# Kernel tuning notes

Hardware: AMD Instinct MI355X
Metric: run time of the kernel (lower is better)

The kernel has to match this reference:

```python
import jax, jax.numpy as jnp
import numpy as np

# dims: N batch, L seq, H heads, d projection_dim, P position_dimension
N, Lq, Lk, H, d, P = 2, 1024, 1024, 8, 64, 1
D = H * d


def _kernel(x):
    # _log_exp_kernel: positive feature map log(1+exp(x)) (softplus)
    return jax.nn.softplus(x)


def setup_inputs() -> dict:
    key = jax.random.key(0)
    ks = jax.random.split(key, 8)
    sc = 1.0 / np.sqrt(D).astype(np.float32)
    return {
        "query": jax.random.normal(ks[0], (N, Lq, D), jnp.float32),
        "key_seq": jax.random.normal(ks[1], (N, Lk, D), jnp.float32),
        "Wq": jax.random.normal(ks[2], (D, D), jnp.float32) * sc,
        "Wk": jax.random.normal(ks[3], (D, D), jnp.float32) * sc,
        "Wv": jax.random.normal(ks[4], (D, D), jnp.float32) * sc,
        "position_coeffs": jax.random.uniform(ks[5], (H, d), jnp.float32, 0.5, 1.5),
        "position_weight": jax.random.normal(ks[6], (H, d, P), jnp.float32) * 1e-3,
        "position_bias": jax.random.normal(ks[7], (H, d), jnp.float32) * 1e-2,
    }


def reference(query, key_seq, Wq, Wk, Wv, position_coeffs, position_weight, position_bias):
    # torch Linear (no bias): y = x @ W.T
    q = _kernel(jnp.einsum('nld,ed->nle', query, Wq).reshape(N, Lq, H, d))
    k = _kernel(jnp.einsum('nld,ed->nle', key_seq, Wk).reshape(N, Lk, H, d))
    v = jnp.einsum('nld,ed->nle', key_seq, Wv).reshape(N, Lk, H, d)
    # (N, H, L, d)
    q = jnp.transpose(q, (0, 2, 1, 3))
    k = jnp.transpose(k, (0, 2, 1, 3))
    v = jnp.transpose(v, (0, 2, 1, 3))

    # default positions: arange, query_offset = 0
    qpos = jnp.broadcast_to(jnp.arange(Lq, dtype=jnp.float32).reshape(1, Lq, 1), (N, Lq, P))
    kpos = jnp.broadcast_to(jnp.arange(Lk, dtype=jnp.float32).reshape(1, Lk, 1), (N, Lk, P))
    pq = jnp.einsum('nlp,hkp->nhlk', qpos, position_weight) + position_bias[None, :, None, :]
    pk = jnp.einsum('nlp,hkp->nhlk', kpos, position_weight)

    coeff = position_coeffs[None, :, None, :]  # (1, H, 1, d)

    def part(f, values):
        # causal (mask_future) linear attention via inclusive cumsum over keys
        Qf = q * f(pq) * coeff           # (N, H, Lq, d)
        Kf = k * f(pk)                   # (N, H, Lk, d)
        S = jnp.cumsum(jnp.einsum('nhkd,nhke->nhkde', Kf, values), axis=2)
        return jnp.einsum('nhqd,nhqde->nhqe', Qf, S)

    num = part(jnp.cos, v) + part(jnp.sin, v)           # (N, H, Lq, d)
    unit = jnp.ones((N, H, Lk, 1), jnp.float32)
    den = part(jnp.cos, unit) + part(jnp.sin, unit)     # (N, H, Lq, 1)
    attn = num / den
    return jnp.transpose(attn, (0, 2, 1, 3)).reshape(N, Lq, D)
```

## Files before the change

kernel.cpp:

```cpp
#include <hip/hip_runtime.h>
#include <cmath>

#define NB    2
#define LSEQ  1024
#define NH    8
#define HD    64
#define DD    512
#define FDIM  128
#define EV    65
#define SEP   80
#define CHUNK 64
#define NC    16
#define NBH   16

typedef short short8 __attribute__((ext_vector_type(8)));
typedef float floatx4 __attribute__((ext_vector_type(4)));
typedef unsigned short ushort;

__device__ __forceinline__ float softplusf(float x) {
  return fmaxf(x, 0.0f) + log1pf(expf(-fabsf(x)));
}

__device__ __forceinline__ ushort f2bf(float f) {
  unsigned u = __float_as_uint(f);
  u += 0x7fffu + ((u >> 16) & 1u);
  return (ushort)(u >> 16);
}

__device__ __forceinline__ short8 cvt8(float4 a, float4 b) {
  short8 r;
  r[0] = (short)f2bf(a.x); r[1] = (short)f2bf(a.y);
  r[2] = (short)f2bf(a.z); r[3] = (short)f2bf(a.w);
  r[4] = (short)f2bf(b.x); r[5] = (short)f2bf(b.y);
  r[6] = (short)f2bf(b.z); r[7] = (short)f2bf(b.w);
  return r;
}

__global__ __launch_bounds__(256) void k_proj(
    const float* __restrict__ Xq, const float* __restrict__ Xkv,
    const float* __restrict__ Wq, const float* __restrict__ Wk,
    const float* __restrict__ Wv, const float* __restrict__ pw,
    const float* __restrict__ pb, const float* __restrict__ pc,
    ushort* __restrict__ Qfb, ushort* __restrict__ Kfb,
    ushort* __restrict__ Vxb)
{
  __shared__ short Al[2][64][72];
  __shared__ short Bl[2][64][72];
  const int b = blockIdx.x;
  int m0, e0, pmode;
  const float *X, *W;
  if (b < 256) {
    m0 = (b >> 3) << 6; e0 = (b & 7) << 6;
    X = Xq; W = Wq + (size_t)e0 * DD; pmode = 0;
  } else {
    const int bb = b - 256;
    m0 = (bb >> 4) << 6;
    const int nt = bb & 15;
    e0 = (nt & 7) << 6;
    X = Xkv;
    if (nt < 8) { W = Wk + (size_t)e0 * DD; pmode = 1; }
    else        { W = Wv + (size_t)e0 * DD; pmode = 2; }
  }
  const int tid  = threadIdx.x;
  const int r    = tid >> 2;
  const int ko   = (tid & 3) << 4;
  const int wave = tid >> 6, lane = tid & 63;
  const int quad = lane >> 4, lm = lane & 15;
  const float* Ag = X + (size_t)(m0 + r) * DD + ko;
  const float* Bg = W + (size_t)r * DD + ko;
  float4 a[4], bb4[4];
#pragma unroll
  for (int u = 0; u < 4; ++u) {
    a[u]   = *(const float4*)(Ag + (u << 2));
    bb4[u] = *(const float4*)(Bg + (u << 2));
  }
  *(short8*)&Al[0][r][ko]     = cvt8(a[0], a[1]);
  *(short8*)&Al[0][r][ko + 8] = cvt8(a[2], a[3]);
  *(short8*)&Bl[0][r][ko]     = cvt8(bb4[0], bb4[1]);
  *(short8*)&Bl[0][r][ko + 8] = cvt8(bb4[2], bb4[3]);
  __syncthreads();

  floatx4 acc[4] = {};
  for (int k0 = 0; k0 < DD; k0 += 64) {
    const int cur  = (k0 >> 6) & 1;
    const bool more = (k0 + 64 < DD);
    if (more) {
#pragma unroll
      for (int u = 0; u < 4; ++u) {
        a[u]   = *(const float4*)(Ag + k0 + 64 + (u << 2));
        bb4[u] = *(const float4*)(Bg + k0 + 64 + (u << 2));
      }
    }
#pragma unroll
    for (int ks = 0; ks < 2; ++ks) {
      const short8 af = *(const short8*)&Al[cur][(wave << 4) + lm][(quad << 3) + (ks << 5)];
#pragma unroll
      for (int t = 0; t < 4; ++t) {
        const short8 bf = *(const short8*)&Bl[cur][(t << 4) + lm][(quad << 3) + (ks << 5)];
        acc[t] = __builtin_amdgcn_mfma_f32_16x16x32_bf16(af, bf, acc[t], 0, 0, 0);
      }
    }
    if (more) {
      const int nxt = cur ^ 1;
      *(short8*)&Al[nxt][r][ko]     = cvt8(a[0], a[1]);
      *(short8*)&Al[nxt][r][ko + 8] = cvt8(a[2], a[3]);
      *(short8*)&Bl[nxt][r][ko]     = cvt8(bb4[0], bb4[1]);
      *(short8*)&Bl[nxt][r][ko + 8] = cvt8(bb4[2], bb4[3]);
    }
    __syncthreads();
  }
#pragma unroll
  for (int t = 0; t < 4; ++t) {
    const int e = e0 + (t << 4) + lm;
    const int h = e >> 6, jj = e & 63;
    if (pmode == 2) {
#pragma unroll
      for (int rg = 0; rg < 4; ++rg) {
        const int m = m0 + (wave << 4) + (quad << 2) + rg;
        const int n = m >> 10, l = m & 1023;
        Vxb[((size_t)(n * NH + h) * LSEQ + l) * HD + jj] = f2bf(acc[t][rg]);
      }
    } else {
      const float pwv = pw[e];
      const float pbv = (pmode == 0) ? pb[e] : 0.0f;
      const float pcv = (pmode == 0) ? pc[e] : 1.0f;
      ushort* base = (pmode == 0) ? Qfb : Kfb;
#pragma unroll
      for (int rg = 0; rg < 4; ++rg) {
        const int m = m0 + (wave << 4) + (quad << 2) + rg;
        const int n = m >> 10, l = m & 1023;
        const float v = softplusf(acc[t][rg]) * pcv;
        const float ang = fmaf((float)l, pwv, pbv);
        ushort* dst = &base[((size_t)(n * NH + h) * LSEQ + l) * FDIM + jj];
        dst[0]  = f2bf(v * __cosf(ang));
        dst[64] = f2bf(v * __sinf(ang));
      }
    }
  }
}

__global__ __launch_bounds__(256) void k_chunk_sums(
    const ushort* __restrict__ Kfb, const ushort* __restrict__ Vxb,
    float* __restrict__ S)
{
  const int blk = blockIdx.x;
  const int bh  = blk >> 5;
  const int c   = (blk >> 1) & (NC - 1);
  const int fh  = blk & 1;
  const int f0  = fh << 6;
  const int t0  = c * CHUNK;
  const int tid  = threadIdx.x;
  const int wave = tid >> 6, lane = tid & 63;
  const int quad = lane >> 4, lm = lane & 15;

  __shared__ short KT[64][72];
  __shared__ short VT[80][72];

  for (int i = tid; i < 64 * 8; i += 256) {
    const int t = i & 63, f8 = (i >> 6) << 3;
    const short8 k8 = *(const short8*)&Kfb[((size_t)bh * LSEQ + t0 + t) * FDIM + f0 + f8];
#pragma unroll
    for (int u = 0; u < 8; ++u) KT[f8 + u][t] = k8[u];
  }
  for (int i = tid; i < 64 * 8; i += 256) {
    const int t = i & 63, e8 = (i >> 6) << 3;
    const short8 v8 = *(const short8*)&Vxb[((size_t)bh * LSEQ + t0 + t) * HD + e8];
#pragma unroll
    for (int u = 0; u < 8; ++u) VT[e8 + u][t] = v8[u];
  }
  if (tid < CHUNK) VT[64][tid] = (short)0x3F80;
  __syncthreads();

  short8 aK[2];
#pragma unroll
  for (int ks = 0; ks < 2; ++ks)
    aK[ks] = *(const short8*)&KT[(wave << 4) + lm][(quad << 3) + (ks << 5)];
  floatx4 acc[5] = {};
#pragma unroll
  for (int nt = 0; nt < 5; ++nt)
#pragma unroll
    for (int ks = 0; ks < 2; ++ks) {
      const short8 bf = *(const short8*)&VT[(nt << 4) + lm][(quad << 3) + (ks << 5)];
      acc[nt] = __builtin_amdgcn_mfma_f32_16x16x32_bf16(aK[ks], bf, acc[nt], 0, 0, 0);
    }

  float* Sb = &S[(size_t)(bh * NC + c) * SEP * FDIM];
#pragma unroll
  for (int nt = 0; nt < 4; ++nt)
#pragma unroll
    for (int rg = 0; rg < 4; ++rg) {
      const int f = f0 + (wave << 4) + (quad << 2) + rg;
      Sb[((nt << 4) + lm) * FDIM + f] = acc[nt][rg];
    }
  if (lm == 0) {
#pragma unroll
    for (int rg = 0; rg < 4; ++rg) {
      const int f = f0 + (wave << 4) + (quad << 2) + rg;
      Sb[64 * FDIM + f] = acc[4][rg];
    }
  }
}

__global__ __launch_bounds__(256) void k_scan(
    const float* __restrict__ S, ushort* __restrict__ PTb)
{
  const int bh = blockIdx.x / 13;
  const int eg = blockIdx.x % 13;
  const size_t cs = (size_t)SEP * FDIM;
  const float* Sg = S + (size_t)bh * NC * cs;
  ushort* Pg = PTb + (size_t)bh * NC * cs;
  for (int i = threadIdx.x; i < 5 * FDIM; i += 256) {
    const int e = eg * 5 + (i >> 7);
    const int f = i & 127;
    const int off = e * FDIM + f;
    float v[NC];
#pragma unroll
    for (int c = 0; c < NC; ++c) v[c] = Sg[(size_t)c * cs + off];
    float s = 0.0f;
#pragma unroll
    for (int c = 0; c < NC; ++c) {
      Pg[(size_t)c * cs + off] = f2bf(s);
      s += v[c];
    }
  }
}

__global__ __launch_bounds__(256) void k_chunk_out(
    const ushort* __restrict__ Qfb, const ushort* __restrict__ Kfb,
    const ushort* __restrict__ Vxb, const ushort* __restrict__ PTb,
    float* __restrict__ Out)
{
  const int c  = blockIdx.x & (NC - 1);
  const int bh = blockIdx.x >> 4;
  const int n  = bh >> 3, h = bh & 7;
  const int t0 = c * CHUNK;
  const int tid  = threadIdx.x;
  const int wave = tid >> 6, lane = tid & 63;
  const int quad = lane >> 4, lm = lane & 15;

  __shared__ short QL[64][128];
  __shared__ short KL[64][128];
  __shared__ short ScL[64][72];
  __shared__ short PT[80][136];
  __shared__ short VT[80][72];
  __shared__ float DenL[64];

  const ushort* Qg = &Qfb[((size_t)bh * LSEQ + t0) * FDIM];
  const ushort* Kg = &Kfb[((size_t)bh * LSEQ + t0) * FDIM];
  for (int i = tid; i < 64 * 16; i += 256) {
    const int r = i >> 4, f8 = (i & 15) << 3;
    *(short8*)&QL[r][f8] = *(const short8*)&Qg[r * FDIM + f8];
    *(short8*)&KL[r][f8] = *(const short8*)&Kg[r * FDIM + f8];
  }
  {
    const ushort* Pg = &PTb[(size_t)(bh * NC + c) * SEP * FDIM];
    for (int i = tid; i < 65 * 16; i += 256) {
      const int e = i >> 4, f8 = (i & 15) << 3;
      *(short8*)&PT[e][f8] = *(const short8*)&Pg[e * FDIM + f8];
    }
  }
  for (int i = tid; i < 64 * 8; i += 256) {
    const int t = i & 63, e8 = (i >> 6) << 3;
    const short8 v8 = *(const short8*)&Vxb[((size_t)bh * LSEQ + t0 + t) * HD + e8];
#pragma unroll
    for (int u = 0; u < 8; ++u) VT[e8 + u][t] = v8[u];
  }
  if (tid < CHUNK) VT[64][tid] = (short)0x3F80;
  __syncthreads();

  short8 aQ[4];
#pragma unroll
  for (int ks = 0; ks < 4; ++ks)
    aQ[ks] = *(const short8*)&QL[(wave << 4) + lm][(quad << 3) + (ks << 5)];

  floatx4 accS[4] = {};
#pragma unroll
  for (int nt = 0; nt < 4; ++nt)
#pragma unroll
    for (int ks = 0; ks < 4; ++ks) {
      const short8 b = *(const short8*)&KL[(nt << 4) + lm][(quad << 3) + (ks << 5)];
      accS[nt] = __builtin_amdgcn_mfma_f32_16x16x32_bf16(aQ[ks], b, accS[nt], 0, 0, 0);
    }
#pragma unroll
  for (int nt = 0; nt < 4; ++nt)
#pragma unroll
    for (int rg = 0; rg < 4; ++rg) {
      const int m = (wave << 4) + (quad << 2) + rg;
      const int t = (nt << 4) + lm;
      ScL[m][t] = (short)((t <= m) ? f2bf(accS[nt][rg]) : 0);
    }

  floatx4 accN[5] = {};
#pragma unroll
  for (int nt = 0; nt < 5; ++nt)
#pragma unroll
    for (int ks = 0; ks < 4; ++ks) {
      const short8 b = *(const short8*)&PT[(nt << 4) + lm][(quad << 3) + (ks << 5)];
      accN[nt] = __builtin_amdgcn_mfma_f32_16x16x32_bf16(aQ[ks], b, accN[nt], 0, 0, 0);
    }

  short8 aS[2];
#pragma unroll
  for (int ks = 0; ks < 2; ++ks)
    aS[ks] = *(const short8*)&ScL[(wave << 4) + lm][(quad << 3) + (ks << 5)];
  floatx4 accV[5] = {};
#pragma unroll
  for (int nt = 0; nt < 5; ++nt)
#pragma unroll
    for (int ks = 0; ks < 2; ++ks) {
      const short8 b = *(const short8*)&VT[(nt << 4) + lm][(quad << 3) + (ks << 5)];
      accV[nt] = __builtin_amdgcn_mfma_f32_16x16x32_bf16(aS[ks], b, accV[nt], 0, 0, 0);
    }

  if (lm == 0) {
#pragma unroll
    for (int rg = 0; rg < 4; ++rg)
      DenL[(wave << 4) + (quad << 2) + rg] = accN[4][rg] + accV[4][rg];
  }

#pragma unroll
  for (int rg = 0; rg < 4; ++rg) {
    const int m = (wave << 4) + (quad << 2) + rg;
    const float rden = 1.0f / DenL[m];
    const int l = t0 + m;
#pragma unroll
    for (int nt = 0; nt < 4; ++nt) {
      const float val = (accN[nt][rg] + accV[nt][rg]) * rden;
      Out[((size_t)(n * LSEQ + l)) * DD + h * HD + (nt << 4) + lm] = val;
    }
  }
}

extern "C" void kernel_launch(void* const* d_in, const int* in_sizes, int n_in,
                              void* d_out, int out_size, void* d_ws, size_t ws_size,
                              hipStream_t stream) {
  (void)in_sizes; (void)n_in; (void)out_size; (void)ws_size;
  const float* query  = (const float*)d_in[0];
  const float* keyseq = (const float*)d_in[1];
  const float* Wq     = (const float*)d_in[2];
  const float* Wk     = (const float*)d_in[3];
  const float* Wv     = (const float*)d_in[4];
  const float* pc     = (const float*)d_in[5];
  const float* pw     = (const float*)d_in[6];
  const float* pb     = (const float*)d_in[7];
  float* out = (float*)d_out;

  ushort* Qfb = (ushort*)d_ws;
  ushort* Kfb = Qfb + (size_t)NBH * LSEQ * FDIM;
  ushort* Vxb = Kfb + (size_t)NBH * LSEQ * FDIM;
  float*  S   = (float*)(Vxb + (size_t)NBH * LSEQ * HD);
  ushort* PTb = (ushort*)(S + (size_t)NBH * NC * SEP * FDIM);

  k_proj      <<<768,          256, 0, stream>>>(query, keyseq, Wq, Wk, Wv, pw, pb, pc, Qfb, Kfb, Vxb);
  k_chunk_sums<<<NBH * NC * 2, 256, 0, stream>>>(Kfb, Vxb, S);
  k_scan      <<<NBH * 13,     256, 0, stream>>>(S, PTb);
  k_chunk_out <<<NBH * NC,     256, 0, stream>>>(Qfb, Kfb, Vxb, PTb, out);
}
```

Before: 112.6 us.

## Fuse four attention kernels into one cooperative kernel with grid syncs

Replaces the four separate launches (projection, chunk sums, scan, chunk output) with a single cooperative kernel of 512 blocks that runs each stage in turn, separated by grid-wide barriers. Shared memory is one union buffer that each stage reinterprets, and the projection stage loops over its 768 tiles. The goal is to remove per-launch overhead and the gaps between kernels. In exchange, the 75KB static shared allocation limits occupancy, the projection now takes two passes over tiles, and each grid sync adds its own barrier cost.

```diff
diff --git a/kernel.cpp b/kernel.cpp
--- a/kernel.cpp
+++ b/kernel.cpp
@@ -1,5 +1,8 @@
 #include <hip/hip_runtime.h>
+#include <hip/hip_cooperative_groups.h>
 #include <cmath>
+
+namespace cg = cooperative_groups;
 
 #define NB    2
 #define LSEQ  1024
@@ -36,297 +39,294 @@
   return r;
 }
 
-__global__ __launch_bounds__(256) void k_proj(
+__global__ __launch_bounds__(256) void k_fused(
     const float* __restrict__ Xq, const float* __restrict__ Xkv,
     const float* __restrict__ Wq, const float* __restrict__ Wk,
     const float* __restrict__ Wv, const float* __restrict__ pw,
     const float* __restrict__ pb, const float* __restrict__ pc,
     ushort* __restrict__ Qfb, ushort* __restrict__ Kfb,
-    ushort* __restrict__ Vxb)
+    ushort* __restrict__ Vxb, float* __restrict__ S,
+    ushort* __restrict__ PTb, float* __restrict__ Out)
 {
-  __shared__ short Al[2][64][72];
-  __shared__ short Bl[2][64][72];
-  const int b = blockIdx.x;
-  int m0, e0, pmode;
-  const float *X, *W;
-  if (b < 256) {
-    m0 = (b >> 3) << 6; e0 = (b & 7) << 6;
-    X = Xq; W = Wq + (size_t)e0 * DD; pmode = 0;
-  } else {
-    const int bb = b - 256;
-    m0 = (bb >> 4) << 6;
-    const int nt = bb & 15;
-    e0 = (nt & 7) << 6;
-    X = Xkv;
-    if (nt < 8) { W = Wk + (size_t)e0 * DD; pmode = 1; }
-    else        { W = Wv + (size_t)e0 * DD; pmode = 2; }
-  }
-  const int tid  = threadIdx.x;
-  const int r    = tid >> 2;
-  const int ko   = (tid & 3) << 4;
-  const int wave = tid >> 6, lane = tid & 63;
-  const int quad = lane >> 4, lm = lane & 15;
-  const float* Ag = X + (size_t)(m0 + r) * DD + ko;
-  const float* Bg = W + (size_t)r * DD + ko;
-  float4 a[4], bb4[4];
-#pragma unroll
-  for (int u = 0; u < 4; ++u) {
-    a[u]   = *(const float4*)(Ag + (u << 2));
-    bb4[u] = *(const float4*)(Bg + (u << 2));
-  }
-  *(short8*)&Al[0][r][ko]     = cvt8(a[0], a[1]);
-  *(short8*)&Al[0][r][ko + 8] = cvt8(a[2], a[3]);
-  *(short8*)&Bl[0][r][ko]     = cvt8(bb4[0], bb4[1]);
-  *(short8*)&Bl[0][r][ko + 8] = cvt8(bb4[2], bb4[3]);
-  __syncthreads();
-
-  floatx4 acc[4] = {};
-  for (int k0 = 0; k0 < DD; k0 += 64) {
-    const int cur  = (k0 >> 6) & 1;
-    const bool more = (k0 + 64 < DD);
-    if (more) {
-#pragma unroll
-      for (int u = 0; u < 4; ++u) {
-        a[u]   = *(const float4*)(Ag + k0 + 64 + (u << 2));
-        bb4[u] = *(const float4*)(Bg + k0 + 64 + (u << 2));
-      }
-    }
-#pragma unroll
-    for (int ks = 0; ks < 2; ++ks) {
-      const short8 af = *(const short8*)&Al[cur][(wave << 4) + lm][(quad << 3) + (ks << 5)];
-#pragma unroll
-      for (int t = 0; t < 4; ++t) {
-        const short8 bf = *(const short8*)&Bl[cur][(t << 4) + lm][(quad << 3) + (ks << 5)];
-        acc[t] = __builtin_amdgcn_mfma_f32_16x16x32_bf16(af, bf, acc[t], 0, 0, 0);
-      }
-    }
-    if (more) {
-      const int nxt = cur ^ 1;
-      *(short8*)&Al[nxt][r][ko]     = cvt8(a[0], a[1]);
-      *(short8*)&Al[nxt][r][ko + 8] = cvt8(a[2], a[3]);
-      *(short8*)&Bl[nxt][r][ko]     = cvt8(bb4[0], bb4[1]);
-      *(short8*)&Bl[nxt][r][ko + 8] = cvt8(bb4[2], bb4[3]);
-    }
-    __syncthreads();
-  }
-#pragma unroll
-  for (int t = 0; t < 4; ++t) {
-    const int e = e0 + (t << 4) + lm;
-    const int h = e >> 6, jj = e & 63;
-    if (pmode == 2) {
-#pragma unroll
-      for (int rg = 0; rg < 4; ++rg) {
-        const int m = m0 + (wave << 4) + (quad << 2) + rg;
-        const int n = m >> 10, l = m & 1023;
-        Vxb[((size_t)(n * NH + h) * LSEQ + l) * HD + jj] = f2bf(acc[t][rg]);
-      }
-    } else {
-      const float pwv = pw[e];
-      const float pbv = (pmode == 0) ? pb[e] : 0.0f;
-      const float pcv = (pmode == 0) ? pc[e] : 1.0f;
-      ushort* base = (pmode == 0) ? Qfb : Kfb;
-#pragma unroll
-      for (int rg = 0; rg < 4; ++rg) {
-        const int m = m0 + (wave << 4) + (quad << 2) + rg;
-        const int n = m >> 10, l = m & 1023;
-        const float v = softplusf(acc[t][rg]) * pcv;
-        const float ang = fmaf((float)l, pwv, pbv);
-        ushort* dst = &base[((size_t)(n * NH + h) * LSEQ + l) * FDIM + jj];
-        dst[0]  = f2bf(v * __cosf(ang));
-        dst[64] = f2bf(v * __sinf(ang));
-      }
-    }
-  }
-}
-
-__global__ __launch_bounds__(256) void k_chunk_sums(
-    const ushort* __restrict__ Kfb, const ushort* __restrict__ Vxb,
-    float* __restrict__ S)
-{
-  const int blk = blockIdx.x;
-  const int bh  = blk >> 5;
-  const int c   = (blk >> 1) & (NC - 1);
-  const int fh  = blk & 1;
-  const int f0  = fh << 6;
-  const int t0  = c * CHUNK;
+  cg::grid_group grid = cg::this_grid();
+  __shared__ __align__(16) char smem[75520];
+
+  const int bid  = blockIdx.x;
   const int tid  = threadIdx.x;
   const int wave = tid >> 6, lane = tid & 63;
   const int quad = lane >> 4, lm = lane & 15;
 
-  __shared__ short KT[64][72];
-  __shared__ short VT[80][72];
-
-  for (int i = tid; i < 64 * 8; i += 256) {
-    const int t = i & 63, f8 = (i >> 6) << 3;
-    const short8 k8 = *(const short8*)&Kfb[((size_t)bh * LSEQ + t0 + t) * FDIM + f0 + f8];
-#pragma unroll
-    for (int u = 0; u < 8; ++u) KT[f8 + u][t] = k8[u];
+  {
+    short (*Al)[64][72] = reinterpret_cast<short (*)[64][72]>(smem);
+    short (*Bl)[64][72] = reinterpret_cast<short (*)[64][72]>(smem + 18432);
+    for (int task = bid; task < 768; task += 512) {
+      int m0, e0, pmode;
+      const float *X, *W;
+      if (task < 256) {
+        m0 = (task >> 3) << 6; e0 = (task & 7) << 6;
+        X = Xq; W = Wq + (size_t)e0 * DD; pmode = 0;
+      } else {
+        const int bb = task - 256;
+        m0 = (bb >> 4) << 6;
+        const int nt = bb & 15;
+        e0 = (nt & 7) << 6;
+        X = Xkv;
+        if (nt < 8) { W = Wk + (size_t)e0 * DD; pmode = 1; }
+        else        { W = Wv + (size_t)e0 * DD; pmode = 2; }
+      }
+      const int r  = tid >> 2;
+      const int ko = (tid & 3) << 4;
+      const float* Ag = X + (size_t)(m0 + r) * DD + ko;
+      const float* Bg = W + (size_t)r * DD + ko;
+      float4 a[4], bb4[4];
+#pragma unroll
+      for (int u = 0; u < 4; ++u) {
+        a[u]   = *(const float4*)(Ag + (u << 2));
+        bb4[u] = *(const float4*)(Bg + (u << 2));
+      }
+      __syncthreads();
+      *(short8*)&Al[0][r][ko]     = cvt8(a[0], a[1]);
+      *(short8*)&Al[0][r][ko + 8] = cvt8(a[2], a[3]);
+      *(short8*)&Bl[0][r][ko]     = cvt8(bb4[0], bb4[1]);
+      *(short8*)&Bl[0][r][ko + 8] = cvt8(bb4[2], bb4[3]);
+      __syncthreads();
+
+      floatx4 acc[4] = {};
+      for (int k0 = 0; k0 < DD; k0 += 64) {
+        const int cur   = (k0 >> 6) & 1;
+        const bool more = (k0 + 64 < DD);
+        if (more) {
+#pragma unroll
+          for (int u = 0; u < 4; ++u) {
+            a[u]   = *(const float4*)(Ag + k0 + 64 + (u << 2));
+            bb4[u] = *(const float4*)(Bg + k0 + 64 + (u << 2));
+          }
+        }
+#pragma unroll
+        for (int ks = 0; ks < 2; ++ks) {
+          const short8 af = *(const short8*)&Al[cur][(wave << 4) + lm][(quad << 3) + (ks << 5)];
+#pragma unroll
+          for (int t = 0; t < 4; ++t) {
+            const short8 bf = *(const short8*)&Bl[cur][(t << 4) + lm][(quad << 3) + (ks << 5)];
+            acc[t] = __builtin_amdgcn_mfma_f32_16x16x32_bf16(af, bf, acc[t], 0, 0, 0);
+          }
+        }
+        if (more) {
+          const int nxt = cur ^ 1;
+          *(short8*)&Al[nxt][r][ko]     = cvt8(a[0], a[1]);
+          *(short8*)&Al[nxt][r][ko + 8] = cvt8(a[2], a[3]);
+          *(short8*)&Bl[nxt][r][ko]     = cvt8(bb4[0], bb4[1]);
+          *(short8*)&Bl[nxt][r][ko + 8] = cvt8(bb4[2], bb4[3]);
+        }
+        __syncthreads();
+      }
+#pragma unroll
+      for (int t = 0; t < 4; ++t) {
+        const int e = e0 + (t << 4) + lm;
+        const int h = e >> 6, jj = e & 63;
+        if (pmode == 2) {
+#pragma unroll
+          for (int rg = 0; rg < 4; ++rg) {
+            const int m = m0 + (wave << 4) + (quad << 2) + rg;
+            const int n = m >> 10, l = m & 1023;
+            Vxb[((size_t)(n * NH + h) * LSEQ + l) * HD + jj] = f2bf(acc[t][rg]);
+          }
+        } else {
+          const float pwv = pw[e];
+          const float pbv = (pmode == 0) ? pb[e] : 0.0f;
+          const float pcv = (pmode == 0) ? pc[e] : 1.0f;
+          ushort* base = (pmode == 0) ? Qfb : Kfb;
+#pragma unroll
+          for (int rg = 0; rg < 4; ++rg) {
+            const int m = m0 + (wave << 4) + (quad << 2) + rg;
+            const int n = m >> 10, l = m & 1023;
+            const float v = softplusf(acc[t][rg]) * pcv;
+            const float ang = fmaf((float)l, pwv, pbv);
+            ushort* dst = &base[((size_t)(n * NH + h) * LSEQ + l) * FDIM + jj];
+            dst[0]  = f2bf(v * __cosf(ang));
+            dst[64] = f2bf(v * __sinf(ang));
+          }
+        }
+      }
+    }
   }
-  for (int i = tid; i < 64 * 8; i += 256) {
-    const int t = i & 63, e8 = (i >> 6) << 3;
-    const short8 v8 = *(const short8*)&Vxb[((size_t)bh * LSEQ + t0 + t) * HD + e8];
-#pragma unroll
-    for (int u = 0; u < 8; ++u) VT[e8 + u][t] = v8[u];
+  grid.sync();
+
+  {
+    short (*KT)[72] = reinterpret_cast<short (*)[72]>(smem);
+    short (*VT)[72] = reinterpret_cast<short (*)[72]>(smem + 9216);
+    const int blk = bid;
+    const int bh  = blk >> 5;
+    const int c   = (blk >> 1) & (NC - 1);
+    const int fh  = blk & 1;
+    const int f0  = fh << 6;
+    const int t0  = c * CHUNK;
+
+    for (int i = tid; i < 64 * 8; i += 256) {
+      const int t = i & 63, f8 = (i >> 6) << 3;
+      const short8 k8 = *(const short8*)&Kfb[((size_t)bh * LSEQ + t0 + t) * FDIM + f0 + f8];
+#pragma unroll
+      for (int u = 0; u < 8; ++u) KT[f8 + u][t] = k8[u];
+    }
+    for (int i = tid; i < 64 * 8; i += 256) {
+      const int t = i & 63, e8 = (i >> 6) << 3;
+      const short8 v8 = *(const short8*)&Vxb[((size_t)bh * LSEQ + t0 + t) * HD + e8];
+#pragma unroll
+      for (int u = 0; u < 8; ++u) VT[e8 + u][t] = v8[u];
+    }
+    if (tid < CHUNK) VT[64][tid] = (short)0x3F80;
+    __syncthreads();
+
+    short8 aK[2];
+#pragma unroll
+    for (int ks = 0; ks < 2; ++ks)
+      aK[ks] = *(const short8*)&KT[(wave << 4) + lm][(quad << 3) + (ks << 5)];
+    floatx4 acc[5] = {};
+#pragma unroll
+    for (int nt = 0; nt < 5; ++nt)
+#pragma unroll
+      for (int ks = 0; ks < 2; ++ks) {
+        const short8 bf = *(const short8*)&VT[(nt << 4) + lm][(quad << 3) + (ks << 5)];
+        acc[nt] = __builtin_amdgcn_mfma_f32_16x16x32_bf16(aK[ks], bf, acc[nt], 0, 0, 0);
+      }
+
+    float* Sb = &S[(size_t)(bh * NC + c) * SEP * FDIM];
+#pragma unroll
+    for (int nt = 0; nt < 4; ++nt)
+#pragma unroll
+      for (int rg = 0; rg < 4; ++rg) {
+        const int f = f0 + (wave << 4) + (quad << 2) + rg;
+        Sb[((nt << 4) + lm) * FDIM + f] = acc[nt][rg];
+      }
+    if (lm == 0) {
+#pragma unroll
+      for (int rg = 0; rg < 4; ++rg) {
+        const int f = f0 + (wave << 4) + (quad << 2) + rg;
+        Sb[64 * FDIM + f] = acc[4][rg];
+      }
+    }
   }
-  if (tid < CHUNK) VT[64][tid] = (short)0x3F80;
-  __syncthreads();
-
-  short8 aK[2];
-#pragma unroll
-  for (int ks = 0; ks < 2; ++ks)
-    aK[ks] = *(const short8*)&KT[(wave << 4) + lm][(quad << 3) + (ks << 5)];
-  floatx4 acc[5] = {};
-#pragma unroll
-  for (int nt = 0; nt < 5; ++nt)
-#pragma unroll
-    for (int ks = 0; ks < 2; ++ks) {
-      const short8 bf = *(const short8*)&VT[(nt << 4) + lm][(quad << 3) + (ks << 5)];
-      acc[nt] = __builtin_amdgcn_mfma_f32_16x16x32_bf16(aK[ks], bf, acc[nt], 0, 0, 0);
-    }
-
-  float* Sb = &S[(size_t)(bh * NC + c) * SEP * FDIM];
-#pragma unroll
-  for (int nt = 0; nt < 4; ++nt)
-#pragma unroll
-    for (int rg = 0; rg < 4; ++rg) {
-      const int f = f0 + (wave << 4) + (quad << 2) + rg;
-      Sb[((nt << 4) + lm) * FDIM + f] = acc[nt][rg];
-    }
-  if (lm == 0) {
-#pragma unroll
-    for (int rg = 0; rg < 4; ++rg) {
-      const int f = f0 + (wave << 4) + (quad << 2) + rg;
-      Sb[64 * FDIM + f] = acc[4][rg];
+  grid.sync();
+
+  if (bid < NBH * 13) {
+    const int bh = bid / 13;
+    const int eg = bid % 13;
+    const size_t cs = (size_t)SEP * FDIM;
+    const float* Sg = S + (size_t)bh * NC * cs;
+    ushort* Pg = PTb + (size_t)bh * NC * cs;
+    for (int i = tid; i < 5 * FDIM; i += 256) {
+      const int e = eg * 5 + (i >> 7);
+      const int f = i & 127;
+      const int off = e * FDIM + f;
+      float v[NC];
+#pragma unroll
+      for (int c = 0; c < NC; ++c) v[c] = Sg[(size_t)c * cs + off];
+      float s = 0.0f;
+#pragma unroll
+      for (int c = 0; c < NC; ++c) {
+        Pg[(size_t)c * cs + off] = f2bf(s);
+        s += v[c];
+      }
     }
   }
-}
-
-__global__ __launch_bounds__(256) void k_scan(
-    const float* __restrict__ S, ushort* __restrict__ PTb)
-{
-  const int bh = blockIdx.x / 13;
-  const int eg = blockIdx.x % 13;
-  const size_t cs = (size_t)SEP * FDIM;
-  const float* Sg = S + (size_t)bh * NC * cs;
-  ushort* Pg = PTb + (size_t)bh * NC * cs;
-  for (int i = threadIdx.x; i < 5 * FDIM; i += 256) {
-    const int e = eg * 5 + (i >> 7);
-    const int f = i & 127;
-    const int off = e * FDIM + f;
-    float v[NC];
-#pragma unroll
-    for (int c = 0; c < NC; ++c) v[c] = Sg[(size_t)c * cs + off];
-    float s = 0.0f;
-#pragma unroll
-    for (int c = 0; c < NC; ++c) {
-      Pg[(size_t)c * cs + off] = f2bf(s);
-      s += v[c];
-    }
-  }
-}
-
-__global__ __launch_bounds__(256) void k_chunk_out(
-    const ushort* __restrict__ Qfb, const ushort* __restrict__ Kfb,
-    const ushort* __restrict__ Vxb, const ushort* __restrict__ PTb,
-    float* __restrict__ Out)
-{
-  const int c  = blockIdx.x & (NC - 1);
-  const int bh = blockIdx.x >> 4;
-  const int n  = bh >> 3, h = bh & 7;
-  const int t0 = c * CHUNK;
-  const int tid  = threadIdx.x;
-  const int wave = tid >> 6, lane = tid & 63;
-  const int quad = lane >> 4, lm = lane & 15;
-
-  __shared__ short QL[64][128];
-  __shared__ short KL[64][128];
-  __shared__ short ScL[64][72];
-  __shared__ short PT[80][136];
-  __shared__ short VT[80][72];
-  __shared__ float DenL[64];
-
-  const ushort* Qg = &Qfb[((size_t)bh * LSEQ + t0) * FDIM];
-  const ushort* Kg = &Kfb[((size_t)bh * LSEQ + t0) * FDIM];
-  for (int i = tid; i < 64 * 16; i += 256) {
-    const int r = i >> 4, f8 = (i & 15) << 3;
-    *(short8*)&QL[r][f8] = *(const short8*)&Qg[r * FDIM + f8];
-    *(short8*)&KL[r][f8] = *(const short8*)&Kg[r * FDIM + f8];
-  }
-  {
-    const ushort* Pg = &PTb[(size_t)(bh * NC + c) * SEP * FDIM];
-    for (int i = tid; i < 65 * 16; i += 256) {
-      const int e = i >> 4, f8 = (i & 15) << 3;
-      *(short8*)&PT[e][f8] = *(const short8*)&Pg[e * FDIM + f8];
-    }
-  }
-  for (int i = tid; i < 64 * 8; i += 256) {
-    const int t = i & 63, e8 = (i >> 6) << 3;
-    const short8 v8 = *(const short8*)&Vxb[((size_t)bh * LSEQ + t0 + t) * HD + e8];
-#pragma unroll
-    for (int u = 0; u < 8; ++u) VT[e8 + u][t] = v8[u];
-  }
-  if (tid < CHUNK) VT[64][tid] = (short)0x3F80;
-  __syncthreads();
-
-  short8 aQ[4];
-#pragma unroll
-  for (int ks = 0; ks < 4; ++ks)
-    aQ[ks] = *(const short8*)&QL[(wave << 4) + lm][(quad << 3) + (ks << 5)];
-
-  floatx4 accS[4] = {};
-#pragma unroll
-  for (int nt = 0; nt < 4; ++nt)
-#pragma unroll
-    for (int ks = 0; ks < 4; ++ks) {
-      const short8 b = *(const short8*)&KL[(nt << 4) + lm][(quad << 3) + (ks << 5)];
-      accS[nt] = __builtin_amdgcn_mfma_f32_16x16x32_bf16(aQ[ks], b, accS[nt], 0, 0, 0);
-    }
-#pragma unroll
-  for (int nt = 0; nt < 4; ++nt)
+  grid.sync();
+
+  if (bid < NBH * NC) {
+    short (*QL)[128]  = reinterpret_cast<short (*)[128]>(smem);
+    short (*KL)[128]  = reinterpret_cast<short (*)[128]>(smem + 16384);
+    short (*ScL)[72]  = reinterpret_cast<short (*)[72]> (smem + 32768);
+    short (*PT)[136]  = reinterpret_cast<short (*)[136]>(smem + 41984);
+    short (*VT)[72]   = reinterpret_cast<short (*)[72]> (smem + 63744);
+    float* DenL       = reinterpret_cast<float*>        (smem + 75264);
+
+    const int c  = bid & (NC - 1);
+    const int bh = bid >> 4;
+    const int n  = bh >> 3, h = bh & 7;
+    const int t0 = c * CHUNK;
+
+    const ushort* Qg = &Qfb[((size_t)bh * LSEQ + t0) * FDIM];
+    const ushort* Kg = &Kfb[((size_t)bh * LSEQ + t0) * FDIM];
+    for (int i = tid; i < 64 * 16; i += 256) {
+      const int r = i >> 4, f8 = (i & 15) << 3;
+      *(short8*)&QL[r][f8] = *(const short8*)&Qg[r * FDIM + f8];
+      *(short8*)&KL[r][f8] = *(const short8*)&Kg[r * FDIM + f8];
+    }
+    {
+      const ushort* Pg = &PTb[(size_t)(bh * NC + c) * SEP * FDIM];
+      for (int i = tid; i < 65 * 16; i += 256) {
+        const int e = i >> 4, f8 = (i & 15) << 3;
+        *(short8*)&PT[e][f8] = *(const short8*)&Pg[e * FDIM + f8];
+      }
+    }
+    for (int i = tid; i < 64 * 8; i += 256) {
+      const int t = i & 63, e8 = (i >> 6) << 3;
+      const short8 v8 = *(const short8*)&Vxb[((size_t)bh * LSEQ + t0 + t) * HD + e8];
+#pragma unroll
+      for (int u = 0; u < 8; ++u) VT[e8 + u][t] = v8[u];
+    }
+    if (tid < CHUNK) VT[64][tid] = (short)0x3F80;
+    __syncthreads();
+
+    short8 aQ[4];
+#pragma unroll
+    for (int ks = 0; ks < 4; ++ks)
+      aQ[ks] = *(const short8*)&QL[(wave << 4) + lm][(quad << 3) + (ks << 5)];
+
+    floatx4 accS[4] = {};
+#pragma unroll
+    for (int nt = 0; nt < 4; ++nt)
+#pragma unroll
+      for (int ks = 0; ks < 4; ++ks) {
+        const short8 b = *(const short8*)&KL[(nt << 4) + lm][(quad << 3) + (ks << 5)];
+        accS[nt] = __builtin_amdgcn_mfma_f32_16x16x32_bf16(aQ[ks], b, accS[nt], 0, 0, 0);
+      }
+#pragma unroll
+    for (int nt = 0; nt < 4; ++nt)
+#pragma unroll
+      for (int rg = 0; rg < 4; ++rg) {
+        const int m = (wave << 4) + (quad << 2) + rg;
+        const int t = (nt << 4) + lm;
+        ScL[m][t] = (short)((t <= m) ? f2bf(accS[nt][rg]) : 0);
+      }
+
+    floatx4 accN[5] = {};
+#pragma unroll
+    for (int nt = 0; nt < 5; ++nt)
+#pragma unroll
+      for (int ks = 0; ks < 4; ++ks) {
+        const short8 b = *(const short8*)&PT[(nt << 4) + lm][(quad << 3) + (ks << 5)];
+        accN[nt] = __builtin_amdgcn_mfma_f32_16x16x32_bf16(aQ[ks], b, accN[nt], 0, 0, 0);
+      }
+
+    short8 aS[2];
+#pragma unroll
+    for (int ks = 0; ks < 2; ++ks)
+      aS[ks] = *(const short8*)&ScL[(wave << 4) + lm][(quad << 3) + (ks << 5)];
+    floatx4 accV[5] = {};
+#pragma unroll
+    for (int nt = 0; nt < 5; ++nt)
+#pragma unroll
+      for (int ks = 0; ks < 2; ++ks) {
+        const short8 b = *(const short8*)&VT[(nt << 4) + lm][(quad << 3) + (ks << 5)];
+        accV[nt] = __builtin_amdgcn_mfma_f32_16x16x32_bf16(aS[ks], b, accV[nt], 0, 0, 0);
+      }
+
+    if (lm == 0) {
+#pragma unroll
+      for (int rg = 0; rg < 4; ++rg)
+        DenL[(wave << 4) + (quad << 2) + rg] = accN[4][rg] + accV[4][rg];
+    }
+
 #pragma unroll
     for (int rg = 0; rg < 4; ++rg) {
       const int m = (wave << 4) + (quad << 2) + rg;
-      const int t = (nt << 4) + lm;
-      ScL[m][t] = (short)((t <= m) ? f2bf(accS[nt][rg]) : 0);
-    }
-
-  floatx4 accN[5] = {};
-#pragma unroll
-  for (int nt = 0; nt < 5; ++nt)
-#pragma unroll
-    for (int ks = 0; ks < 4; ++ks) {
-      const short8 b = *(const short8*)&PT[(nt << 4) + lm][(quad << 3) + (ks << 5)];
-      accN[nt] = __builtin_amdgcn_mfma_f32_16x16x32_bf16(aQ[ks], b, accN[nt], 0, 0, 0);
-    }
-
-  short8 aS[2];
-#pragma unroll
-  for (int ks = 0; ks < 2; ++ks)
-    aS[ks] = *(const short8*)&ScL[(wave << 4) + lm][(quad << 3) + (ks << 5)];
-  floatx4 accV[5] = {};
-#pragma unroll
-  for (int nt = 0; nt < 5; ++nt)
-#pragma unroll
-    for (int ks = 0; ks < 2; ++ks) {
-      const short8 b = *(const short8*)&VT[(nt << 4) + lm][(quad << 3) + (ks << 5)];
-      accV[nt] = __builtin_amdgcn_mfma_f32_16x16x32_bf16(aS[ks], b, accV[nt], 0, 0, 0);
-    }
-
-  if (lm == 0) {
-#pragma unroll
-    for (int rg = 0; rg < 4; ++rg)
-      DenL[(wave << 4) + (quad << 2) + rg] = accN[4][rg] + accV[4][rg];
-  }
-
-#pragma unroll
-  for (int rg = 0; rg < 4; ++rg) {
-    const int m = (wave << 4) + (quad << 2) + rg;
-    const float rden = 1.0f / DenL[m];
-    const int l = t0 + m;
-#pragma unroll
-    for (int nt = 0; nt < 4; ++nt) {
-      const float val = (accN[nt][rg] + accV[nt][rg]) * rden;
-      Out[((size_t)(n * LSEQ + l)) * DD + h * HD + (nt << 4) + lm] = val;
+      const float rden = 1.0f / DenL[m];
+      const int l = t0 + m;
+#pragma unroll
+      for (int nt = 0; nt < 4; ++nt) {
+        const float val = (accN[nt][rg] + accV[nt][rg]) * rden;
+        Out[((size_t)(n * LSEQ + l)) * DD + h * HD + (nt << 4) + lm] = val;
+      }
     }
   }
 }
@@ -351,8 +351,10 @@
   float*  S   = (float*)(Vxb + (size_t)NBH * LSEQ * HD);
   ushort* PTb = (ushort*)(S + (size_t)NBH * NC * SEP * FDIM);
 
-  k_proj      <<<768,          256, 0, stream>>>(query, keyseq, Wq, Wk, Wv, pw, pb, pc, Qfb, Kfb, Vxb);
-  k_chunk_sums<<<NBH * NC * 2, 256, 0, stream>>>(Kfb, Vxb, S);
-  k_scan      <<<NBH * 13,     256, 0, stream>>>(S, PTb);
-  k_chunk_out <<<NBH * NC,     256, 0, stream>>>(Qfb, Kfb, Vxb, PTb, out);
-}
+  void* args[] = {
+    (void*)&query, (void*)&keyseq, (void*)&Wq, (void*)&Wk, (void*)&Wv,
+    (void*)&pw, (void*)&pb, (void*)&pc,
+    (void*)&Qfb, (void*)&Kfb, (void*)&Vxb, (void*)&S, (void*)&PTb, (void*)&out
+  };
+  hipLaunchCooperativeKernel((void*)k_fused, dim3(512), dim3(256), args, 0, stream);
+}
```

Result: slower. 305.6 us (+171.4%).
